# Optimization experiments

Measured on AMD Instinct MI355X. Metric: run time of the kernel, lower is better.

## Reference

```python
import jax, jax.numpy as jnp
import numpy as np

N_STEPS = 3            # n_internal_steps
USE_CURRENT_ACTIVS = True
LEAKY_SLOPE = 0.01     # F.leaky_relu default


def _apply_act(x, ids):
    # per-node activation lookup: 0=identity 1=leaky_relu 2=relu 3=sigmoid 4=tanh
    return jnp.select(
        [ids == 0, ids == 1, ids == 2, ids == 3],
        [x,
         jnp.where(x >= 0, x, LEAKY_SLOPE * x),
         jnp.maximum(x, jnp.zeros((), x.dtype)),
         jax.nn.sigmoid(x)],
        jnp.tanh(x))


def setup_inputs() -> dict:
    key = jax.random.key(0)
    ks = jax.random.split(key, 14)
    B, NI, NH, NO = 1, 4096, 8192, 2048
    s = 0.02  # keep recurrent dynamics stable
    return {
        "inputs": jax.random.normal(ks[0], (B, NI), jnp.float32),
        "W_i2h": jax.random.normal(ks[1], (NH, NI), jnp.float32) * s,
        "W_h2h": jax.random.normal(ks[2], (NH, NH), jnp.float32) * s,
        "W_o2h": jax.random.normal(ks[3], (NH, NO), jnp.float32) * s,
        "W_i2o": jax.random.normal(ks[4], (NO, NI), jnp.float32) * s,
        "W_h2o": jax.random.normal(ks[5], (NO, NH), jnp.float32) * s,
        "W_o2o": jax.random.normal(ks[6], (NO, NO), jnp.float32) * s,
        "hidden_responses": jax.random.uniform(ks[7], (NH,), jnp.float32, 0.5, 1.5),
        "hidden_biases": jax.random.normal(ks[8], (NH,), jnp.float32) * 0.1,
        "output_responses": jax.random.uniform(ks[9], (NO,), jnp.float32, 0.5, 1.5),
        "output_biases": jax.random.normal(ks[10], (NO,), jnp.float32) * 0.1,
        "activs0": jnp.zeros((B, NH), jnp.float32),
        "outputs0": jnp.zeros((B, NO), jnp.float32),
        "hidden_act_ids": jax.random.randint(ks[11], (NH,), 0, 5, jnp.int32),
        "output_act_ids": jax.random.randint(ks[12], (NO,), 0, 5, jnp.int32),
    }


def reference(inputs, W_i2h, W_h2h, W_o2h, W_i2o, W_h2o, W_o2o,
              hidden_responses, hidden_biases, output_responses, output_biases,
              activs0, outputs0, hidden_act_ids, output_act_ids):
    activs = activs0          # (B, NH) recurrent hidden state
    outputs = outputs0        # (B, NO) recurrent output state
    activs_for_output = activs
    for _ in range(N_STEPS):
        pre = hidden_responses * (inputs @ W_i2h.T
                                  + activs @ W_h2h.T
                                  + outputs @ W_o2h.T) + hidden_biases
        activs = _apply_act(pre, hidden_act_ids[None, :])
    if USE_CURRENT_ACTIVS:
        activs_for_output = activs
    out_in = inputs @ W_i2o.T + outputs @ W_o2o.T + activs_for_output @ W_h2o.T
    pre_out = output_responses * out_in + output_biases
    return _apply_act(pre_out, output_act_ids[None, :])
```

## Files before the change

### kernel.cpp

```cpp
#include <hip/hip_runtime.h>

#define NI 4096
#define NH 8192
#define NO 2048

typedef float  f4 __attribute__((ext_vector_type(4)));
typedef unsigned short u16x8 __attribute__((ext_vector_type(8)));
typedef unsigned int   u32x2 __attribute__((ext_vector_type(2)));

__device__ __forceinline__ float apply_act(float x, int id) {
    switch (id) {
        case 0:  return x;
        case 1:  return x >= 0.f ? x : 0.01f * x;
        case 2:  return fmaxf(x, 0.f);
        case 3:  return 1.f / (1.f + expf(-x));
        default: return tanhf(x);
    }
}

__device__ __forceinline__ unsigned int f2bf(float f) {
    unsigned int u = __float_as_uint(f);
    return (u + 0x7FFFu + ((u >> 16) & 1u)) >> 16;
}
__device__ __forceinline__ float bf2f(unsigned int b) {
    return __uint_as_float(b << 16);
}

template <bool NT>
__device__ __forceinline__ float wave_dot(const float* __restrict__ Wrow,
                                          const float* __restrict__ x,
                                          int K, int lane) {
    const f4* __restrict__ W4 = (const f4*)Wrow;
    const f4* __restrict__ x4 = (const f4*)x;
    float acc = 0.f;
    const int n4 = K >> 2;
    #pragma unroll 4
    for (int i = lane; i < n4; i += 64) {
        f4 w = NT ? __builtin_nontemporal_load(W4 + i) : W4[i];
        f4 v = x4[i];
        acc = fmaf(w.x, v.x, acc);
        acc = fmaf(w.y, v.y, acc);
        acc = fmaf(w.z, v.z, acc);
        acc = fmaf(w.w, v.w, acc);
    }
    #pragma unroll
    for (int off = 32; off; off >>= 1) acc += __shfl_xor(acc, off, 64);
    return acc;
}

__device__ __forceinline__ float wave_dot_bf(const unsigned short* __restrict__ Wrow,
                                             const float* __restrict__ x,
                                             int K, int lane) {
    const u16x8* __restrict__ W8 = (const u16x8*)Wrow;
    const f4* __restrict__ x4 = (const f4*)x;
    float acc = 0.f;
    const int n8 = K >> 3;
    #pragma unroll 4
    for (int i = lane; i < n8; i += 64) {
        u16x8 w = W8[i];
        f4 va = x4[2 * i];
        f4 vb = x4[2 * i + 1];
        acc = fmaf(bf2f(w[0]), va.x, acc);
        acc = fmaf(bf2f(w[1]), va.y, acc);
        acc = fmaf(bf2f(w[2]), va.z, acc);
        acc = fmaf(bf2f(w[3]), va.w, acc);
        acc = fmaf(bf2f(w[4]), vb.x, acc);
        acc = fmaf(bf2f(w[5]), vb.y, acc);
        acc = fmaf(bf2f(w[6]), vb.z, acc);
        acc = fmaf(bf2f(w[7]), vb.w, acc);
    }
    #pragma unroll
    for (int off = 32; off; off >>= 1) acc += __shfl_xor(acc, off, 64);
    return acc;
}

__global__ __launch_bounds__(256) void k_flags(const float* __restrict__ xin,
                                               const float* __restrict__ a0,
                                               const float* __restrict__ o0,
                                               int* __restrict__ flags) {
    __shared__ int s[3];
    int t = threadIdx.x;
    if (t < 3) s[t] = 0;
    __syncthreads();
    int f0 = 0, f1 = 0, f2 = 0;
    for (int i = t; i < NI; i += 256) f0 |= (xin[i] != 0.f);
    for (int i = t; i < NH; i += 256) f1 |= (a0[i]  != 0.f);
    for (int i = t; i < NO; i += 256) f2 |= (o0[i]  != 0.f);
    if (f0) atomicOr(&s[0], 1);
    if (f1) atomicOr(&s[1], 1);
    if (f2) atomicOr(&s[2], 1);
    __syncthreads();
    if (t < 3) flags[t] = s[t];
}

__global__ __launch_bounds__(256) void k_h_init(const float* __restrict__ W_i2h,
                                                const float* __restrict__ W_o2h,
                                                const float* __restrict__ W_h2h,
                                                const float* __restrict__ xin,
                                                const float* __restrict__ o0,
                                                const float* __restrict__ a0,
                                                const float* __restrict__ resp,
                                                const float* __restrict__ bias,
                                                const int* __restrict__ ids,
                                                const int* __restrict__ flags,
                                                float* __restrict__ c_h,
                                                float* __restrict__ act_a) {
    int wave = threadIdx.x >> 6;
    int lane = threadIdx.x & 63;
    int m = blockIdx.x * 4 + wave;
    float c = 0.f;
    if (flags[0]) c += wave_dot<true>(W_i2h + (size_t)m * NI, xin, NI, lane);
    if (flags[2]) c += wave_dot<true>(W_o2h + (size_t)m * NO, o0,  NO, lane);
    float d = 0.f;
    if (flags[1]) d = wave_dot<false>(W_h2h + (size_t)m * NH, a0, NH, lane);
    if (lane == 0) {
        c_h[m] = c;
        act_a[m] = apply_act(fmaf(resp[m], c + d, bias[m]), ids[m]);
    }
}

__global__ __launch_bounds__(256) void k_step2_conv(const float* __restrict__ W_h2h,
                                                    const float* __restrict__ x,
                                                    const float* __restrict__ c_h,
                                                    const float* __restrict__ resp,
                                                    const float* __restrict__ bias,
                                                    const int* __restrict__ ids,
                                                    float* __restrict__ out,
                                                    unsigned short* __restrict__ Wb) {
    int wave = threadIdx.x >> 6;
    int lane = threadIdx.x & 63;
    int m = blockIdx.x * 4 + wave;
    const f4* __restrict__ W4 = (const f4*)(W_h2h + (size_t)m * NH);
    const f4* __restrict__ x4 = (const f4*)x;
    u32x2* __restrict__ B2 = (u32x2*)(Wb + (size_t)m * NH);
    float acc = 0.f;
    #pragma unroll 4
    for (int i = lane; i < NH / 4; i += 64) {
        f4 w = __builtin_nontemporal_load(W4 + i);
        f4 v = x4[i];
        acc = fmaf(w.x, v.x, acc);
        acc = fmaf(w.y, v.y, acc);
        acc = fmaf(w.z, v.z, acc);
        acc = fmaf(w.w, v.w, acc);
        u32x2 b;
        b.x = f2bf(w.x) | (f2bf(w.y) << 16);
        b.y = f2bf(w.z) | (f2bf(w.w) << 16);
        B2[i] = b;
    }
    #pragma unroll
    for (int off = 32; off; off >>= 1) acc += __shfl_xor(acc, off, 64);
    if (lane == 0) {
        float pre = fmaf(resp[m], c_h[m] + acc, bias[m]);
        out[m] = apply_act(pre, ids[m]);
    }
}

__global__ __launch_bounds__(256) void k_step3_bf(const unsigned short* __restrict__ Wb,
                                                  const float* __restrict__ x,
                                                  const float* __restrict__ c_h,
                                                  const float* __restrict__ resp,
                                                  const float* __restrict__ bias,
                                                  const int* __restrict__ ids,
                                                  float* __restrict__ out) {
    int wave = threadIdx.x >> 6;
    int lane = threadIdx.x & 63;
    int m = (NH - 1) - (blockIdx.x * 4 + wave);
    float dot = wave_dot_bf(Wb + (size_t)m * NH, x, NH, lane);
    if (lane == 0) {
        float pre = fmaf(resp[m], c_h[m] + dot, bias[m]);
        out[m] = apply_act(pre, ids[m]);
    }
}

template <int REV>
__global__ __launch_bounds__(256) void k_step(const float* __restrict__ W_h2h,
                                              const float* __restrict__ x,
                                              const float* __restrict__ c_h,
                                              const float* __restrict__ resp,
                                              const float* __restrict__ bias,
                                              const int* __restrict__ ids,
                                              float* __restrict__ out) {
    int wave = threadIdx.x >> 6;
    int lane = threadIdx.x & 63;
    int m = blockIdx.x * 4 + wave;
    if (REV) m = (NH - 1) - m;
    float dot = wave_dot<false>(W_h2h + (size_t)m * NH, x, NH, lane);
    if (lane == 0) {
        float pre = fmaf(resp[m], c_h[m] + dot, bias[m]);
        out[m] = apply_act(pre, ids[m]);
    }
}

__global__ __launch_bounds__(256) void k_final(const float* __restrict__ W_i2o,
                                               const float* __restrict__ W_o2o,
                                               const float* __restrict__ W_h2o,
                                               const float* __restrict__ xin,
                                               const float* __restrict__ o0,
                                               const float* __restrict__ act,
                                               const float* __restrict__ resp,
                                               const float* __restrict__ bias,
                                               const int* __restrict__ ids,
                                               const int* __restrict__ flags,
                                               float* __restrict__ out) {
    int wave = threadIdx.x >> 6;
    int lane = threadIdx.x & 63;
    int m = blockIdx.x * 4 + wave;
    float dot = wave_dot<true>(W_h2o + (size_t)m * NH, act, NH, lane);
    if (flags[0]) dot += wave_dot<true>(W_i2o + (size_t)m * NI, xin, NI, lane);
    if (flags[2]) dot += wave_dot<true>(W_o2o + (size_t)m * NO, o0,  NO, lane);
    if (lane == 0) {
        float pre = fmaf(resp[m], dot, bias[m]);
        out[m] = apply_act(pre, ids[m]);
    }
}

extern "C" void kernel_launch(void* const* d_in, const int* in_sizes, int n_in,
                              void* d_out, int out_size, void* d_ws, size_t ws_size,
                              hipStream_t stream) {
    const float* inputs   = (const float*)d_in[0];
    const float* W_i2h    = (const float*)d_in[1];
    const float* W_h2h    = (const float*)d_in[2];
    const float* W_o2h    = (const float*)d_in[3];
    const float* W_i2o    = (const float*)d_in[4];
    const float* W_h2o    = (const float*)d_in[5];
    const float* W_o2o    = (const float*)d_in[6];
    const float* h_resp   = (const float*)d_in[7];
    const float* h_bias   = (const float*)d_in[8];
    const float* o_resp   = (const float*)d_in[9];
    const float* o_bias   = (const float*)d_in[10];
    const float* activs0  = (const float*)d_in[11];
    const float* outputs0 = (const float*)d_in[12];
    const int*   h_ids    = (const int*)d_in[13];
    const int*   o_ids    = (const int*)d_in[14];

    float* ws    = (float*)d_ws;
    float* c_h   = ws;
    float* act_a = ws + NH;
    float* act_b = ws + 2 * NH;
    int*   flags = (int*)(ws + 3 * NH);

    size_t bf_off = (((size_t)(3 * NH + 4) * sizeof(float)) + 255) & ~(size_t)255;
    unsigned short* Wb = (unsigned short*)((char*)d_ws + bf_off);
    bool use_bf = ws_size >= bf_off + (size_t)NH * NH * sizeof(unsigned short);

    k_flags<<<1, 256, 0, stream>>>(inputs, activs0, outputs0, flags);

    k_h_init<<<NH / 4, 256, 0, stream>>>(W_i2h, W_o2h, W_h2h, inputs, outputs0,
                                         activs0, h_resp, h_bias, h_ids, flags,
                                         c_h, act_a);
    if (use_bf) {
        k_step2_conv<<<NH / 4, 256, 0, stream>>>(W_h2h, act_a, c_h, h_resp, h_bias,
                                                 h_ids, act_b, Wb);
        k_step3_bf<<<NH / 4, 256, 0, stream>>>(Wb, act_b, c_h, h_resp, h_bias,
                                               h_ids, act_a);
    } else {
        k_step<0><<<NH / 4, 256, 0, stream>>>(W_h2h, act_a, c_h, h_resp, h_bias,
                                              h_ids, act_b);
        k_step<1><<<NH / 4, 256, 0, stream>>>(W_h2h, act_b, c_h, h_resp, h_bias,
                                              h_ids, act_a);
    }

    k_final<<<NO / 4, 256, 0, stream>>>(W_i2o, W_o2o, W_h2o, inputs, outputs0, act_a,
                                        o_resp, o_bias, o_ids, flags, (float*)d_out);
}
```

Before: 143.3 us.

## Convert W_h2h to bf16 in the init kernel and run both later steps in bf16

Moves the fp32-to-bf16 conversion of W_h2h into the first hidden-state kernel. That kernel now always streams W_h2h, computing its dot product and writing the bf16 copy. Both remaining recurrent steps then read only the bf16 weights, which halves their weight traffic. The catch is that the init kernel previously skipped W_h2h entirely when activs0 is all zero, so this adds a full fp32 read plus a bf16 write there. It also lowers step 2 from fp32 to bf16 precision.

```diff
diff --git a/kernel.cpp b/kernel.cpp
--- a/kernel.cpp
+++ b/kernel.cpp
@@ -93,6 +93,71 @@
     if (t < 3) flags[t] = s[t];
 }
 
+__global__ __launch_bounds__(256) void k_h_init_conv(const float* __restrict__ W_i2h,
+                                                     const float* __restrict__ W_o2h,
+                                                     const float* __restrict__ W_h2h,
+                                                     const float* __restrict__ xin,
+                                                     const float* __restrict__ o0,
+                                                     const float* __restrict__ a0,
+                                                     const float* __restrict__ resp,
+                                                     const float* __restrict__ bias,
+                                                     const int* __restrict__ ids,
+                                                     const int* __restrict__ flags,
+                                                     float* __restrict__ c_h,
+                                                     float* __restrict__ act_a,
+                                                     unsigned short* __restrict__ Wb) {
+    int wave = threadIdx.x >> 6;
+    int lane = threadIdx.x & 63;
+    int m = blockIdx.x * 4 + wave;
+
+    const f4* __restrict__ W4 = (const f4*)(W_h2h + (size_t)m * NH);
+    const f4* __restrict__ a4 = (const f4*)a0;
+    u32x2* __restrict__ B2 = (u32x2*)(Wb + (size_t)m * NH);
+    float d = 0.f;
+    #pragma unroll 4
+    for (int i = lane; i < NH / 4; i += 64) {
+        f4 w = __builtin_nontemporal_load(W4 + i);
+        f4 v = a4[i];
+        d = fmaf(w.x, v.x, d);
+        d = fmaf(w.y, v.y, d);
+        d = fmaf(w.z, v.z, d);
+        d = fmaf(w.w, v.w, d);
+        u32x2 b;
+        b.x = f2bf(w.x) | (f2bf(w.y) << 16);
+        b.y = f2bf(w.z) | (f2bf(w.w) << 16);
+        B2[i] = b;
+    }
+    #pragma unroll
+    for (int off = 32; off; off >>= 1) d += __shfl_xor(d, off, 64);
+
+    float c = 0.f;
+    if (flags[0]) c += wave_dot<true>(W_i2h + (size_t)m * NI, xin, NI, lane);
+    if (flags[2]) c += wave_dot<true>(W_o2h + (size_t)m * NO, o0,  NO, lane);
+
+    if (lane == 0) {
+        c_h[m] = c;
+        float dd = flags[1] ? d : 0.f;
+        act_a[m] = apply_act(fmaf(resp[m], c + dd, bias[m]), ids[m]);
+    }
+}
+
+__global__ __launch_bounds__(256) void k_step_bf(const unsigned short* __restrict__ Wb,
+                                                 const float* __restrict__ x,
+                                                 const float* __restrict__ c_h,
+                                                 const float* __restrict__ resp,
+                                                 const float* __restrict__ bias,
+                                                 const int* __restrict__ ids,
+                                                 float* __restrict__ out) {
+    int wave = threadIdx.x >> 6;
+    int lane = threadIdx.x & 63;
+    int m = blockIdx.x * 4 + wave;
+    float dot = wave_dot_bf(Wb + (size_t)m * NH, x, NH, lane);
+    if (lane == 0) {
+        float pre = fmaf(resp[m], c_h[m] + dot, bias[m]);
+        out[m] = apply_act(pre, ids[m]);
+    }
+}
+
 __global__ __launch_bounds__(256) void k_h_init(const float* __restrict__ W_i2h,
                                                 const float* __restrict__ W_o2h,
                                                 const float* __restrict__ W_h2h,
@@ -116,59 +181,6 @@
     if (lane == 0) {
         c_h[m] = c;
         act_a[m] = apply_act(fmaf(resp[m], c + d, bias[m]), ids[m]);
-    }
-}
-
-__global__ __launch_bounds__(256) void k_step2_conv(const float* __restrict__ W_h2h,
-                                                    const float* __restrict__ x,
-                                                    const float* __restrict__ c_h,
-                                                    const float* __restrict__ resp,
-                                                    const float* __restrict__ bias,
-                                                    const int* __restrict__ ids,
-                                                    float* __restrict__ out,
-                                                    unsigned short* __restrict__ Wb) {
-    int wave = threadIdx.x >> 6;
-    int lane = threadIdx.x & 63;
-    int m = blockIdx.x * 4 + wave;
-    const f4* __restrict__ W4 = (const f4*)(W_h2h + (size_t)m * NH);
-    const f4* __restrict__ x4 = (const f4*)x;
-    u32x2* __restrict__ B2 = (u32x2*)(Wb + (size_t)m * NH);
-    float acc = 0.f;
-    #pragma unroll 4
-    for (int i = lane; i < NH / 4; i += 64) {
-        f4 w = __builtin_nontemporal_load(W4 + i);
-        f4 v = x4[i];
-        acc = fmaf(w.x, v.x, acc);
-        acc = fmaf(w.y, v.y, acc);
-        acc = fmaf(w.z, v.z, acc);
-        acc = fmaf(w.w, v.w, acc);
-        u32x2 b;
-        b.x = f2bf(w.x) | (f2bf(w.y) << 16);
-        b.y = f2bf(w.z) | (f2bf(w.w) << 16);
-        B2[i] = b;
-    }
-    #pragma unroll
-    for (int off = 32; off; off >>= 1) acc += __shfl_xor(acc, off, 64);
-    if (lane == 0) {
-        float pre = fmaf(resp[m], c_h[m] + acc, bias[m]);
-        out[m] = apply_act(pre, ids[m]);
-    }
-}
-
-__global__ __launch_bounds__(256) void k_step3_bf(const unsigned short* __restrict__ Wb,
-                                                  const float* __restrict__ x,
-                                                  const float* __restrict__ c_h,
-                                                  const float* __restrict__ resp,
-                                                  const float* __restrict__ bias,
-                                                  const int* __restrict__ ids,
-                                                  float* __restrict__ out) {
-    int wave = threadIdx.x >> 6;
-    int lane = threadIdx.x & 63;
-    int m = (NH - 1) - (blockIdx.x * 4 + wave);
-    float dot = wave_dot_bf(Wb + (size_t)m * NH, x, NH, lane);
-    if (lane == 0) {
-        float pre = fmaf(resp[m], c_h[m] + dot, bias[m]);
-        out[m] = apply_act(pre, ids[m]);
     }
 }
 
@@ -245,15 +257,18 @@
 
     k_flags<<<1, 256, 0, stream>>>(inputs, activs0, outputs0, flags);
 
-    k_h_init<<<NH / 4, 256, 0, stream>>>(W_i2h, W_o2h, W_h2h, inputs, outputs0,
-                                         activs0, h_resp, h_bias, h_ids, flags,
-                                         c_h, act_a);
     if (use_bf) {
-        k_step2_conv<<<NH / 4, 256, 0, stream>>>(W_h2h, act_a, c_h, h_resp, h_bias,
-                                                 h_ids, act_b, Wb);
-        k_step3_bf<<<NH / 4, 256, 0, stream>>>(Wb, act_b, c_h, h_resp, h_bias,
-                                               h_ids, act_a);
+        k_h_init_conv<<<NH / 4, 256, 0, stream>>>(W_i2h, W_o2h, W_h2h, inputs,
+                                                  outputs0, activs0, h_resp, h_bias,
+                                                  h_ids, flags, c_h, act_a, Wb);
+        k_step_bf<<<NH / 4, 256, 0, stream>>>(Wb, act_a, c_h, h_resp, h_bias,
+                                              h_ids, act_b);
+        k_step_bf<<<NH / 4, 256, 0, stream>>>(Wb, act_b, c_h, h_resp, h_bias,
+                                              h_ids, act_a);
     } else {
+        k_h_init<<<NH / 4, 256, 0, stream>>>(W_i2h, W_o2h, W_h2h, inputs, outputs0,
+                                             activs0, h_resp, h_bias, h_ids, flags,
+                                             c_h, act_a);
         k_step<0><<<NH / 4, 256, 0, stream>>>(W_h2h, act_a, c_h, h_resp, h_bias,
                                               h_ids, act_b);
         k_step<1><<<NH / 4, 256, 0, stream>>>(W_h2h, act_b, c_h, h_resp, h_bias,
```

New measurement: 169.1 us. 18.0% more time.
